# Kernel tuning notes

Hardware: AMD Instinct MI355X
Metric: run time of the kernel (lower is better)

## Reference

```python
import jax, jax.numpy as jnp
import numpy as np

DIGITS = 4
SAMPLES = 2048
BATCH = 512
ALPHA = 0.1


def setup_inputs() -> dict:
    key = jax.random.key(0)
    k1, k2, k3 = jax.random.split(key, 3)
    n1_logits = jax.random.normal(k1, (BATCH, DIGITS, 10), dtype=jnp.float32)
    # sample counters start at ones and stay positive; keep them in (1, 2)
    counters = jax.random.uniform(k2, (DIGITS, 10), dtype=jnp.float32) + 1.0
    s = jax.random.randint(k3, (BATCH,), 0, 10 ** DIGITS, dtype=jnp.int32)
    return {"n1_logits": n1_logits, "counters": counters, "s": s}


def reference(n1_logits, counters, s):
    B, D, _ = n1_logits.shape
    S = SAMPLES
    key = jax.random.key(42)
    digit_idx = jnp.arange(10, dtype=jnp.int32)
    constraint = jnp.zeros((B, S), dtype=jnp.int32)
    samples_list = []
    for i in range(D):
        if i == 0:
            maxim = (s // 10 ** (D - 1)).astype(jnp.int32)
            minim = jnp.maximum(0, maxim - 9)
        else:
            maxim = ((s // 10 ** (D - 1 - i)) % 10).astype(jnp.int32)
            minim = jnp.zeros_like(maxim)
        # [B, S, 10]: per-digit logits repeated over samples, counter penalty
        probs = n1_logits[:, i, None, :] - ALPHA * jnp.log(counters[i])[None, None, :]
        probs = jnp.broadcast_to(probs, (B, S, 10))
        # restrict to [minim, maxim] per batch row (equiv of per-row tf.concat with -inf pads)
        valid = (digit_idx[None, :] >= minim[:, None]) & (digit_idx[None, :] <= maxim[:, None])  # [B,10]
        probs_cut = jnp.where(valid[:, None, :], probs, -jnp.inf)
        logits = jnp.where(constraint[..., None] == 1, probs, probs_cut)
        key, sub = jax.random.split(key)
        samp = jax.random.categorical(sub, logits).astype(jnp.int32)  # [B,S]
        constraint = jnp.maximum(jnp.where(samp == maxim[:, None], 0, 1), constraint)
        samples_list.append(samp)
    n1_samples = jnp.stack(samples_list, axis=-1)  # [B,S,D]
    multiplier = (10 ** jnp.arange(D - 1, -1, -1)).astype(jnp.int32)  # [D]
    n1_summed = jnp.sum(n1_samples * multiplier, axis=-1)  # [B,S]
    n2 = s[:, None] - n1_summed  # [B,S], guaranteed in [0, 10^D)
    # sample_weights: per-row multiplicity of each sampled value (unique_with_counts+gather)
    V = 10 ** D
    row = jnp.arange(B, dtype=jnp.int32)[:, None]
    hist = jnp.zeros((B, V), jnp.float32).at[row, n1_summed].add(1.0)
    weights = jnp.take_along_axis(hist, n1_summed, axis=1)  # [B,S]
    # decimalise n2 via cumulative-quotient + sorted shift trick (faithful to tf code)
    mult2 = jnp.concatenate(
        [jnp.full((D - 1,), 10, dtype=jnp.int32), jnp.zeros((1,), dtype=jnp.int32)]
    )  # [10,...,10,0]
    n2d = n2[..., None] // multiplier  # [B,S,D] cumulative quotients
    n2d = n2d - jnp.sort(n2d * mult2, axis=-1)
    return n1_samples[..., None], n2d[..., None], weights
```

## Files before the change

kernel.cpp:

```cpp
#include <hip/hip_runtime.h>
#include <stdint.h>
#include <stddef.h>


namespace {

constexpr int B = 512, S = 2048, D = 4, NC = 10;
constexpr int BS = B * S;
constexpr size_t OUT1_OFF = (size_t)BS * D;
constexpr size_t OUT2_OFF = (size_t)BS * D * 2;

constexpr uint32_t crotl(uint32_t x, int d) { return (x << d) | (x >> (32 - d)); }
struct CU2 { uint32_t a, b; };
constexpr CU2 ctf(uint32_t k0, uint32_t k1, uint32_t c0, uint32_t c1) {
  uint32_t ks2 = k0 ^ k1 ^ 0x1BD11BDAu;
  uint32_t x0 = c0 + k0, x1 = c1 + k1;
  const int rots[8] = {13, 15, 26, 6, 17, 29, 16, 24};
  const uint32_t ks[3] = {k0, k1, ks2};
  for (int blk = 0; blk < 5; ++blk) {
    for (int j = 0; j < 4; ++j) {
      int r = rots[(blk & 1) * 4 + j];
      x0 += x1; x1 = crotl(x1, r); x1 ^= x0;
    }
    x0 += ks[(blk + 1) % 3];
    x1 += ks[(blk + 2) % 3] + (uint32_t)(blk + 1);
  }
  return CU2{x0, x1};
}

struct Keys { uint32_t kx[D]; uint32_t ky[D]; };
constexpr Keys make_keys() {
  Keys K{};
  uint32_t a = 0u, b = 42u;
  for (int i = 0; i < D; ++i) {
    CU2 sub = ctf(a, b, 0u, 1u);
    CU2 nk  = ctf(a, b, 0u, 0u);
    K.kx[i] = sub.a; K.ky[i] = sub.b;
    a = nk.a; b = nk.b;
  }
  return K;
}
constexpr Keys KEYS = make_keys();

__device__ __forceinline__ uint32_t rotl32(uint32_t x, int d) {
  return (x << d) | (x >> (32 - d));
}
template <uint32_t K0, uint32_t K1>
__device__ __forceinline__ uint32_t tf_xor(uint32_t c1) {
  constexpr uint32_t KS2 = K0 ^ K1 ^ 0x1BD11BDAu;
  uint32_t x0 = K0, x1 = c1 + K1;
#define TF_RND(r) { x0 += x1; x1 = rotl32(x1, (r)); x1 ^= x0; }
  TF_RND(13) TF_RND(15) TF_RND(26) TF_RND(6)   x0 += K1;  x1 += KS2 + 1u;
  TF_RND(17) TF_RND(29) TF_RND(16) TF_RND(24)  x0 += KS2; x1 += K0 + 2u;
  TF_RND(13) TF_RND(15) TF_RND(26) TF_RND(6)   x0 += K0;  x1 += K1 + 3u;
  TF_RND(17) TF_RND(29) TF_RND(16) TF_RND(24)  x0 += K1;  x1 += KS2 + 4u;
  TF_RND(13) TF_RND(15) TF_RND(26) TF_RND(6)   x0 += KS2; x1 += K0 + 5u;
#undef TF_RND
  return x0 ^ x1;
}

__device__ __forceinline__ float xla_logf(float a) {
  uint32_t bits = __float_as_uint(a);
  float e = (float)((int)(bits >> 23) - 126);
  float m = __uint_as_float((bits & 0x007fffffu) | 0x3f000000u);
  bool mlt = m < 0.707106781186547524f;
  float tmp = mlt ? m : 0.0f;
  float x = __fsub_rn(m, 1.0f);
  e = __fsub_rn(e, mlt ? 1.0f : 0.0f);
  x = __fadd_rn(x, tmp);
  float x2 = __fmul_rn(x, x);
  float x3 = __fmul_rn(x2, x);
  float y  = __fmaf_rn(7.0376836292e-2f,  x, -1.1514610310e-1f);
  float y1 = __fmaf_rn(-1.2420140846e-1f, x,  1.4249322787e-1f);
  float y2 = __fmaf_rn(2.0000714765e-1f,  x, -2.4999993993e-1f);
  y  = __fmaf_rn(y,  x,  1.1676998740e-1f);
  y1 = __fmaf_rn(y1, x, -1.6668057665e-1f);
  y2 = __fmaf_rn(y2, x,  3.3333331174e-1f);
  y  = __fmaf_rn(y, x3, y1);
  y  = __fmaf_rn(y, x3, y2);
  y  = __fmul_rn(y, x3);
  y1 = __fmul_rn(e, -2.12194440e-4f);
  tmp = __fmul_rn(x2, 0.5f);
  y = __fadd_rn(y, y1);
  x = __fsub_rn(x, tmp);
  y2 = __fmul_rn(e, 0.693359375f);
  x = __fadd_rn(x, y);
  x = __fadd_rn(x, y2);
  return x;
}

__device__ __forceinline__ float gumbel_from_bits(uint32_t bits) {
  float f = __fsub_rn(__uint_as_float((bits >> 9) | 0x3f800000u), 1.0f);
  float u = __fadd_rn(f, 1.17549435e-38f);
  float l1 = xla_logf(u);
  float l2 = xla_logf(-l1);
  return -l2;
}

__device__ __forceinline__ float sgpr_f(float x) {
  return __uint_as_float(__builtin_amdgcn_readfirstlane(__float_as_uint(x)));
}

template <int I>
__device__ __forceinline__ void do_digit(const float* s_p, uint32_t n0,
                                         const int* mx, int& con, int* dg) {
  uint32_t rb[NC];
#pragma unroll
  for (int c = 0; c < NC; ++c)
    rb[c] = tf_xor<KEYS.kx[I], KEYS.ky[I]>(n0 + (uint32_t)c);
  float sp[NC];
#pragma unroll
  for (int c = 0; c < NC; ++c) sp[c] = sgpr_f(s_p[I * NC + c]);
  const int mxi = mx[I];
  float best = -__builtin_inff();
  int bi = 0;
#pragma unroll
  for (int c = 0; c < NC; ++c) {
    float g = gumbel_from_bits(rb[c]);
    float v = __fadd_rn(g, sp[c]);
    bool allowed = (con != 0) || (c <= mxi);
    if (allowed && v > best) { best = v; bi = c; }
  }
  dg[I] = bi;
  con |= (bi != mxi);
}

__global__ __launch_bounds__(256) void sample_kernel(
    const float* __restrict__ logits,
    const float* __restrict__ counters,
    const int*   __restrict__ s_in,
    float* __restrict__ out,
    int*   __restrict__ n1buf,
    int    write_ws)
{
  __shared__ float s_p[D * NC];
  const int t = threadIdx.x;
  const int blk = blockIdx.x;
  const int b = blk >> 3;
  if (t < D * NC) {
    s_p[t] = __fsub_rn(logits[b * D * NC + t],
                       __fmul_rn(0.1f, xla_logf(counters[t])));
  }
  __syncthreads();

  const int tid = blk * 256 + t;
  const int sval = s_in[b];
  const int mx[D] = {sval / 1000, (sval / 100) % 10, (sval / 10) % 10, sval % 10};

  const uint32_t n0 = (uint32_t)tid * (uint32_t)NC;
  int con = 0;
  int dg[D];
  do_digit<0>(s_p, n0, mx, con, dg);
  do_digit<1>(s_p, n0, mx, con, dg);
  do_digit<2>(s_p, n0, mx, con, dg);
  do_digit<3>(s_p, n0, mx, con, dg);

  const int n1v = dg[0] * 1000 + dg[1] * 100 + dg[2] * 10 + dg[3];
  const int n2 = sval - n1v;
  const int q0 = n2 / 1000, q1 = (n2 / 100) % 10, q2 = (n2 / 10) % 10, q3 = n2 % 10;

  const size_t o = (size_t)tid * D;
  *reinterpret_cast<float4*>(out + o) =
      make_float4((float)dg[0], (float)dg[1], (float)dg[2], (float)dg[3]);
  *reinterpret_cast<float4*>(out + OUT1_OFF + o) =
      make_float4((float)q0, (float)q1, (float)q2, (float)q3);
  if (write_ws) n1buf[tid] = n1v;
}

template <bool FROM_WS>
__global__ __launch_bounds__(256) void weights_kernel(
    const int* __restrict__ n1buf, float* __restrict__ out) {
  __shared__ int hist[10000];
  const int t = threadIdx.x;
  const int b = blockIdx.x;
  for (int i = t; i < 10000; i += 256) hist[i] = 0;
  __syncthreads();
  int vals[8];
#pragma unroll
  for (int k = 0; k < 8; ++k) {
    const int sidx = t + k * 256;
    int v;
    if (FROM_WS) {
      v = n1buf[b * S + sidx];
    } else {
      const float* p = out + ((size_t)(b * S + sidx)) * D;
      v = 1000 * (int)p[0] + 100 * (int)p[1] + 10 * (int)p[2] + (int)p[3];
    }
    vals[k] = v;
    atomicAdd(&hist[v], 1);
  }
  __syncthreads();
#pragma unroll
  for (int k = 0; k < 8; ++k) {
    const int sidx = t + k * 256;
    out[OUT2_OFF + (size_t)b * S + sidx] = (float)hist[vals[k]];
  }
}

}

extern "C" void kernel_launch(void* const* d_in, const int* in_sizes, int n_in,
                              void* d_out, int out_size, void* d_ws, size_t ws_size,
                              hipStream_t stream) {
  const float* logits   = (const float*)d_in[0];
  const float* counters = (const float*)d_in[1];
  const int*   s_in     = (const int*)d_in[2];
  float* out = (float*)d_out;
  int*   n1buf = (int*)d_ws;
  const int use_ws = (d_ws != nullptr && ws_size >= (size_t)BS * sizeof(int)) ? 1 : 0;

  sample_kernel<<<BS / 256, 256, 0, stream>>>(logits, counters, s_in, out,
                                              n1buf, use_ws);
  if (use_ws) weights_kernel<true><<<B, 256, 0, stream>>>(n1buf, out);
  else        weights_kernel<false><<<B, 256, 0, stream>>>(nullptr, out);
}
```

Measured before the change: 180.3 us.

## Split sampling into two kernel variants: two-samples-per-thread and rolled-loop with digit-0 skip

The single sampling kernel becomes two kernels, each covering half the samples. The first processes two samples per thread with interleaved Threefry and log work to raise instruction-level parallelism. The second uses a rolled per-class loop and skips classes above the first digit's maximum, cutting RNG and log work for digit 0. Both drop the readfirstlane scalar loads and fold the Gumbel negation into a subtraction. The extra kernel launch and the mix of two code shapes may cancel some of the gains, and the rolled loop loses unrolled ILP.

```diff
diff --git a/kernel.cpp b/kernel.cpp
--- a/kernel.cpp
+++ b/kernel.cpp
@@ -89,81 +89,138 @@
   return x;
 }
 
-__device__ __forceinline__ float gumbel_from_bits(uint32_t bits) {
+__device__ __forceinline__ float l2_of(uint32_t bits) {
   float f = __fsub_rn(__uint_as_float((bits >> 9) | 0x3f800000u), 1.0f);
   float u = __fadd_rn(f, 1.17549435e-38f);
   float l1 = xla_logf(u);
-  float l2 = xla_logf(-l1);
-  return -l2;
-}
-
-__device__ __forceinline__ float sgpr_f(float x) {
-  return __uint_as_float(__builtin_amdgcn_readfirstlane(__float_as_uint(x)));
+  return xla_logf(-l1);
 }
 
 template <int I>
-__device__ __forceinline__ void do_digit(const float* s_p, uint32_t n0,
-                                         const int* mx, int& con, int* dg) {
-  uint32_t rb[NC];
-#pragma unroll
-  for (int c = 0; c < NC; ++c)
-    rb[c] = tf_xor<KEYS.kx[I], KEYS.ky[I]>(n0 + (uint32_t)c);
-  float sp[NC];
-#pragma unroll
-  for (int c = 0; c < NC; ++c) sp[c] = sgpr_f(s_p[I * NC + c]);
-  const int mxi = mx[I];
-  float best = -__builtin_inff();
-  int bi = 0;
+__device__ __forceinline__ void do_digit2(const float* s_p,
+                                          uint32_t n0a, uint32_t n0b, int mxi,
+                                          int& conA, int& conB,
+                                          int& dgA, int& dgB) {
+  uint32_t ra[NC], rb[NC];
 #pragma unroll
   for (int c = 0; c < NC; ++c) {
-    float g = gumbel_from_bits(rb[c]);
-    float v = __fadd_rn(g, sp[c]);
-    bool allowed = (con != 0) || (c <= mxi);
-    if (allowed && v > best) { best = v; bi = c; }
-  }
-  dg[I] = bi;
-  con |= (bi != mxi);
-}
-
-__global__ __launch_bounds__(256) void sample_kernel(
-    const float* __restrict__ logits,
-    const float* __restrict__ counters,
-    const int*   __restrict__ s_in,
-    float* __restrict__ out,
-    int*   __restrict__ n1buf,
-    int    write_ws)
+    ra[c] = tf_xor<KEYS.kx[I], KEYS.ky[I]>(n0a + (uint32_t)c);
+    rb[c] = tf_xor<KEYS.kx[I], KEYS.ky[I]>(n0b + (uint32_t)c);
+  }
+  float la[NC], lb[NC];
+#pragma unroll
+  for (int c = 0; c < NC; ++c) {
+    la[c] = l2_of(ra[c]);
+    lb[c] = l2_of(rb[c]);
+  }
+  float bestA = -__builtin_inff(), bestB = -__builtin_inff();
+  int biA = 0, biB = 0;
+#pragma unroll
+  for (int c = 0; c < NC; ++c) {
+    float sp = s_p[I * NC + c];
+    float vA = __fsub_rn(sp, la[c]);
+    float vB = __fsub_rn(sp, lb[c]);
+    bool okA = (conA != 0) || (c <= mxi);
+    bool okB = (conB != 0) || (c <= mxi);
+    if (okA && vA > bestA) { bestA = vA; biA = c; }
+    if (okB && vB > bestB) { bestB = vB; biB = c; }
+  }
+  dgA = biA; dgB = biB;
+  conA |= (biA != mxi); conB |= (biB != mxi);
+}
+
+__global__ __launch_bounds__(256, 4) void sample_A(
+    const float* __restrict__ logits, const float* __restrict__ counters,
+    const int* __restrict__ s_in, float* __restrict__ out,
+    int* __restrict__ n1buf, int write_ws)
 {
   __shared__ float s_p[D * NC];
   const int t = threadIdx.x;
   const int blk = blockIdx.x;
-  const int b = blk >> 3;
-  if (t < D * NC) {
+  const int b = blk >> 2;
+  if (t < D * NC)
     s_p[t] = __fsub_rn(logits[b * D * NC + t],
                        __fmul_rn(0.1f, xla_logf(counters[t])));
-  }
-  __syncthreads();
-
-  const int tid = blk * 256 + t;
+  __syncthreads();
+
+  const int sidx0 = blk * 512 + 2 * t;
   const int sval = s_in[b];
   const int mx[D] = {sval / 1000, (sval / 100) % 10, (sval / 10) % 10, sval % 10};
-
-  const uint32_t n0 = (uint32_t)tid * (uint32_t)NC;
-  int con = 0;
-  int dg[D];
-  do_digit<0>(s_p, n0, mx, con, dg);
-  do_digit<1>(s_p, n0, mx, con, dg);
-  do_digit<2>(s_p, n0, mx, con, dg);
-  do_digit<3>(s_p, n0, mx, con, dg);
+  const uint32_t n0a = (uint32_t)sidx0 * NC, n0b = n0a + NC;
+
+  int conA = 0, conB = 0, dgA[D], dgB[D];
+  do_digit2<0>(s_p, n0a, n0b, mx[0], conA, conB, dgA[0], dgB[0]);
+  do_digit2<1>(s_p, n0a, n0b, mx[1], conA, conB, dgA[1], dgB[1]);
+  do_digit2<2>(s_p, n0a, n0b, mx[2], conA, conB, dgA[2], dgB[2]);
+  do_digit2<3>(s_p, n0a, n0b, mx[3], conA, conB, dgA[3], dgB[3]);
+
+#pragma unroll
+  for (int k = 0; k < 2; ++k) {
+    const int* dg = k ? dgB : dgA;
+    const int sidx = sidx0 + k;
+    const int n1v = dg[0] * 1000 + dg[1] * 100 + dg[2] * 10 + dg[3];
+    const int n2 = sval - n1v;
+    const size_t o = (size_t)sidx * D;
+    *reinterpret_cast<float4*>(out + o) =
+        make_float4((float)dg[0], (float)dg[1], (float)dg[2], (float)dg[3]);
+    *reinterpret_cast<float4*>(out + OUT1_OFF + o) =
+        make_float4((float)(n2 / 1000), (float)((n2 / 100) % 10),
+                    (float)((n2 / 10) % 10), (float)(n2 % 10));
+    if (write_ws) n1buf[sidx] = n1v;
+  }
+}
+
+template <int I>
+__device__ __forceinline__ void digitB(const float* s_p, uint32_t n0, int mxi,
+                                       int& con, int& dg) {
+  float best = -__builtin_inff();
+  int bi = 0;
+  const int lim = (I == 0) ? mxi : (NC - 1);
+#pragma unroll 1
+  for (int c = 0; c <= lim; ++c) {
+    uint32_t rbits = tf_xor<KEYS.kx[I], KEYS.ky[I]>(n0 + (uint32_t)c);
+    float l2 = l2_of(rbits);
+    float v = __fsub_rn(s_p[I * NC + c], l2);
+    bool allowed = (I == 0) || (con != 0) || (c <= mxi);
+    if (allowed && v > best) { best = v; bi = c; }
+  }
+  dg = bi;
+  con |= (bi != mxi);
+}
+
+__global__ __launch_bounds__(256, 4) void sample_B(
+    const float* __restrict__ logits, const float* __restrict__ counters,
+    const int* __restrict__ s_in, float* __restrict__ out,
+    int* __restrict__ n1buf, int write_ws)
+{
+  __shared__ float s_p[D * NC];
+  const int t = threadIdx.x;
+  const int blk = blockIdx.x;
+  const int tid = BS / 2 + blk * 256 + t;
+  const int b = tid >> 11;
+  if (t < D * NC)
+    s_p[t] = __fsub_rn(logits[b * D * NC + t],
+                       __fmul_rn(0.1f, xla_logf(counters[t])));
+  __syncthreads();
+
+  const int sval = s_in[b];
+  const int mx[D] = {sval / 1000, (sval / 100) % 10, (sval / 10) % 10, sval % 10};
+  const uint32_t n0 = (uint32_t)tid * NC;
+
+  int con = 0, dg[D];
+  digitB<0>(s_p, n0, mx[0], con, dg[0]);
+  digitB<1>(s_p, n0, mx[1], con, dg[1]);
+  digitB<2>(s_p, n0, mx[2], con, dg[2]);
+  digitB<3>(s_p, n0, mx[3], con, dg[3]);
 
   const int n1v = dg[0] * 1000 + dg[1] * 100 + dg[2] * 10 + dg[3];
   const int n2 = sval - n1v;
-  const int q0 = n2 / 1000, q1 = (n2 / 100) % 10, q2 = (n2 / 10) % 10, q3 = n2 % 10;
-
   const size_t o = (size_t)tid * D;
   *reinterpret_cast<float4*>(out + o) =
       make_float4((float)dg[0], (float)dg[1], (float)dg[2], (float)dg[3]);
   *reinterpret_cast<float4*>(out + OUT1_OFF + o) =
-      make_float4((float)q0, (float)q1, (float)q2, (float)q3);
+      make_float4((float)(n2 / 1000), (float)((n2 / 100) % 10),
+                  (float)((n2 / 10) % 10), (float)(n2 % 10));
   if (write_ws) n1buf[tid] = n1v;
 }
 
@@ -209,8 +266,8 @@
   int*   n1buf = (int*)d_ws;
   const int use_ws = (d_ws != nullptr && ws_size >= (size_t)BS * sizeof(int)) ? 1 : 0;
 
-  sample_kernel<<<BS / 256, 256, 0, stream>>>(logits, counters, s_in, out,
-                                              n1buf, use_ws);
+  sample_A<<<1024, 256, 0, stream>>>(logits, counters, s_in, out, n1buf, use_ws);
+  sample_B<<<2048, 256, 0, stream>>>(logits, counters, s_in, out, n1buf, use_ws);
   if (use_ws) weights_kernel<true><<<B, 256, 0, stream>>>(n1buf, out);
   else        weights_kernel<false><<<B, 256, 0, stream>>>(nullptr, out);
 }
```

New measurement: 194.8 us. 8.0% more time.

## Skip first-digit RNG for impossible classes and split sampling into four launches

Applied to the files above, without the earlier changes.

The first digit is now sampled with a uniform per-block bound, held in a scalar register, so Threefry and both logs are only computed for classes up to that digit's maximum. Classes above the maximum can never win, so this removes wasted RNG and log work. The negation of the Gumbel term is folded into a subtraction. The sampling grid is also split into four sequential launches of 1024 blocks each, which adds launch overhead with no obvious benefit.

```diff
diff --git a/kernel.cpp b/kernel.cpp
--- a/kernel.cpp
+++ b/kernel.cpp
@@ -9,6 +9,7 @@
 constexpr int BS = B * S;
 constexpr size_t OUT1_OFF = (size_t)BS * D;
 constexpr size_t OUT2_OFF = (size_t)BS * D * 2;
+constexpr int QBLOCKS = 1024;
 
 constexpr uint32_t crotl(uint32_t x, int d) { return (x << d) | (x >> (32 - d)); }
 struct CU2 { uint32_t a, b; };
@@ -89,12 +90,11 @@
   return x;
 }
 
-__device__ __forceinline__ float gumbel_from_bits(uint32_t bits) {
+__device__ __forceinline__ float l2_of(uint32_t bits) {
   float f = __fsub_rn(__uint_as_float((bits >> 9) | 0x3f800000u), 1.0f);
   float u = __fadd_rn(f, 1.17549435e-38f);
   float l1 = xla_logf(u);
-  float l2 = xla_logf(-l1);
-  return -l2;
+  return xla_logf(-l1);
 }
 
 __device__ __forceinline__ float sgpr_f(float x) {
@@ -116,13 +116,33 @@
   int bi = 0;
 #pragma unroll
   for (int c = 0; c < NC; ++c) {
-    float g = gumbel_from_bits(rb[c]);
-    float v = __fadd_rn(g, sp[c]);
+    float l2 = l2_of(rb[c]);
+    float v = __fsub_rn(sp[c], l2);
     bool allowed = (con != 0) || (c <= mxi);
     if (allowed && v > best) { best = v; bi = c; }
   }
   dg[I] = bi;
   con |= (bi != mxi);
+}
+
+__device__ __forceinline__ void do_digit0(const float* s_p, uint32_t n0,
+                                          int mx0, int& con, int* dg) {
+  const int m0 = __builtin_amdgcn_readfirstlane(mx0);
+  float sp[NC];
+#pragma unroll
+  for (int c = 0; c < NC; ++c) sp[c] = sgpr_f(s_p[c]);
+  float best = __fsub_rn(sp[0], l2_of(tf_xor<KEYS.kx[0], KEYS.ky[0]>(n0)));
+  int bi = 0;
+#pragma unroll
+  for (int c = 1; c < NC; ++c) {
+    if (m0 >= c) {
+      float l2 = l2_of(tf_xor<KEYS.kx[0], KEYS.ky[0]>(n0 + (uint32_t)c));
+      float v = __fsub_rn(sp[c], l2);
+      if (v > best) { best = v; bi = c; }
+    }
+  }
+  dg[0] = bi;
+  con |= (bi != mx0);
 }
 
 __global__ __launch_bounds__(256) void sample_kernel(
@@ -131,26 +151,26 @@
     const int*   __restrict__ s_in,
     float* __restrict__ out,
     int*   __restrict__ n1buf,
-    int    write_ws)
+    int    write_ws, int qi)
 {
   __shared__ float s_p[D * NC];
   const int t = threadIdx.x;
-  const int blk = blockIdx.x;
-  const int b = blk >> 3;
+  const int gblk = qi * QBLOCKS + blockIdx.x;
+  const int b = gblk >> 3;
   if (t < D * NC) {
     s_p[t] = __fsub_rn(logits[b * D * NC + t],
                        __fmul_rn(0.1f, xla_logf(counters[t])));
   }
   __syncthreads();
 
-  const int tid = blk * 256 + t;
+  const int tid = gblk * 256 + t;
   const int sval = s_in[b];
   const int mx[D] = {sval / 1000, (sval / 100) % 10, (sval / 10) % 10, sval % 10};
 
   const uint32_t n0 = (uint32_t)tid * (uint32_t)NC;
   int con = 0;
   int dg[D];
-  do_digit<0>(s_p, n0, mx, con, dg);
+  do_digit0(s_p, n0, mx[0], con, dg);
   do_digit<1>(s_p, n0, mx, con, dg);
   do_digit<2>(s_p, n0, mx, con, dg);
   do_digit<3>(s_p, n0, mx, con, dg);
@@ -209,8 +229,9 @@
   int*   n1buf = (int*)d_ws;
   const int use_ws = (d_ws != nullptr && ws_size >= (size_t)BS * sizeof(int)) ? 1 : 0;
 
-  sample_kernel<<<BS / 256, 256, 0, stream>>>(logits, counters, s_in, out,
-                                              n1buf, use_ws);
+  for (int qi = 0; qi < 4; ++qi)
+    sample_kernel<<<QBLOCKS, 256, 0, stream>>>(logits, counters, s_in, out,
+                                               n1buf, use_ws, qi);
   if (use_ws) weights_kernel<true><<<B, 256, 0, stream>>>(n1buf, out);
   else        weights_kernel<false><<<B, 256, 0, stream>>>(nullptr, out);
 }
```

Result: slower. 190.2 us (+5.5%).
